# Optimization experiments

Measured on AMD Instinct MI355X. Metric: run time of the kernel, lower is better.

Reference implementation:

```python
import jax, jax.numpy as jnp
import numpy as np

T, B, E, H, R, NHASH, CHUNK = 2048, 2, 1024, 8, 2, 8, 32
D = E // H
INF = 1.0e16  # module's self.inf
BIG = 1.0e8   # module's self.big


def setup_inputs() -> dict:
    key = jax.random.key(0)
    ks = jax.random.split(key, 8)
    w = lambda k, shape, s=0.02: jax.random.normal(k, shape, dtype=jnp.float32) * s
    return {
        "query": jax.random.normal(ks[0], (T, B, E), jnp.float32),
        "key":   jax.random.normal(ks[1], (T, B, E), jnp.float32),
        "value": jax.random.normal(ks[2], (T, B, E), jnp.float32),
        "Wq": w(ks[3], (E, E)), "bq": jnp.zeros((E,), jnp.float32),
        "Wv": w(ks[4], (E, E)), "bv": jnp.zeros((E,), jnp.float32),
        "Wo": w(ks[5], (E, E)), "bo": jnp.zeros((E,), jnp.float32),
        "hash_w": w(ks[6], (R, H, D, NHASH // 2), 0.1),
    }


def _hashes(x_tbhd, hash_w):
    # einsum('ibnf,rnfh->ibrnh'), cat([lin,-lin]), argmax -> [T,B,R,H]
    lin = jnp.einsum('tbhd,rhdn->tbrhn', x_tbhd, hash_w)
    return jnp.argmax(jnp.concatenate([lin, -lin], axis=-1), axis=-1)


def _gather_t(x_bhtd, perm_brht):
    # gather along T with per-(b,r,h) permutation -> [B,R,H,T,D]
    Bb, Rr, Hh, Tt = perm_brht.shape
    Dd = x_bhtd.shape[-1]
    xb = jnp.broadcast_to(x_bhtd[:, None], (Bb, Rr, Hh, Tt, Dd))
    idx = jnp.broadcast_to(perm_brht[..., None], (Bb, Rr, Hh, Tt, Dd))
    return jnp.take_along_axis(xb, idx, axis=3)


def reference(query, key, value, Wq, bq, Wv, bv, Wo, bo, hash_w):
    del key  # share_kq=True (self-attention): keys are L2-normalized queries
    scaling = D ** -0.5
    qf = query @ Wq + bq                                    # [T,B,E]
    kf = qf / jnp.linalg.norm(qf, axis=-1, keepdims=True)   # F.normalize over embed dim
    vf = value @ Wv + bv
    q = qf.reshape(T, B, H, D) * scaling
    k = kf.reshape(T, B, H, D)
    v = vf.reshape(T, B, H, D)

    q_hash = _hashes(q, hash_w)                             # [T,B,R,H]
    k_hash = _hashes(k, hash_w)

    qh_t = jnp.transpose(q_hash, (1, 2, 3, 0))              # [B,R,H,T]
    kh_t = jnp.transpose(k_hash, (1, 2, 3, 0))
    p_q = jnp.argsort(qh_t, axis=-1)                        # stable sort by hash
    p_k = jnp.argsort(kh_t, axis=-1)
    inv_q = jnp.argsort(p_q, axis=-1)                       # sorted position of each token

    q_s = _gather_t(jnp.transpose(q, (1, 2, 0, 3)), p_q)    # [B,R,H,T,D]
    k_s = _gather_t(jnp.transpose(k, (1, 2, 0, 3)), p_k)
    v_s = _gather_t(jnp.transpose(v, (1, 2, 0, 3)), p_k)
    qh_s = jnp.take_along_axis(qh_t, p_q, axis=-1)
    kh_s = jnp.take_along_axis(kh_t, p_k, axis=-1)

    C = T // CHUNK
    M = 3 * CHUNK
    chunk = lambda x: x.reshape(x.shape[:3] + (C, CHUNK) + x.shape[4:])
    q_c, qh_c, qid_c = chunk(q_s), chunk(qh_s), chunk(p_q)
    k_c, v_c, kh_c, kid_c = chunk(k_s), chunk(v_s), chunk(kh_s), chunk(p_k)

    # each query chunk attends key chunks {c-1, c, c+1} (num_chunk_offsets=3, wraparound)
    blocks = lambda x: jnp.concatenate([jnp.roll(x, 1, axis=3), x, jnp.roll(x, -1, axis=3)], axis=4)
    kb, vb, khb, kidb = blocks(k_c), blocks(v_c), blocks(kh_c), blocks(kid_c)

    scores = jnp.einsum('brhcld,brhcmd->brhclm', q_c, kb)   # q pre-scaled by d^-0.5
    scores = scores - INF * (qh_c[..., :, None] != khb[..., None, :])   # mask_different_hashes
    scores = scores - BIG * (qid_c[..., :, None] == kidb[..., None, :]) # mask_current

    # cross-round duplicate counting: key ids attended per original query
    chunk_of = inv_q // CHUNK                               # [B,R,H,T]
    idx = jnp.broadcast_to(chunk_of[..., None], (B, R, H, T, M))
    A = jnp.take_along_axis(kidb, idx, axis=3)              # [B,R,H,T,M]
    dup = []
    for r in range(R):
        c = jnp.zeros((B, H, T, M), jnp.int32)
        for r2 in range(R):
            c = c + (A[:, r, :, :, :, None] == A[:, r2, :, :, None, :]).sum(-1, dtype=jnp.int32)
        dup.append(c)
    dup = jnp.stack(dup, axis=1)                            # [B,R,H,T,M]
    idx2 = jnp.broadcast_to(p_q[..., None], (B, R, H, T, M))
    dup_s = jnp.take_along_axis(dup, idx2, axis=3)          # sorted-query order
    scores = scores - jnp.log(dup_s.astype(scores.dtype)).reshape(scores.shape)

    z = jax.nn.logsumexp(scores, axis=-1)                   # [B,R,H,C,L]
    attn = jax.nn.softmax(scores, axis=-1)
    o = jnp.einsum('brhclm,brhcmd->brhcld', attn, vb).reshape(B, R, H, T, D)
    z = z.reshape(B, R, H, T)

    # scatter back to original token order
    idx3 = jnp.broadcast_to(inv_q[..., None], (B, R, H, T, D))
    o = jnp.take_along_axis(o, idx3, axis=3)
    z = jnp.take_along_axis(z, inv_q, axis=3)

    w = jax.nn.softmax(z, axis=1)                           # combine rounds by logsumexp weight
    out = (w[..., None] * o).sum(axis=1)                    # [B,H,T,D]
    out = jnp.transpose(out, (2, 0, 1, 3)).reshape(T, B, E)
    return out @ Wo + bo
```

## Files before the change

### kernel.cpp

```cpp
#include <hip/hip_runtime.h>

typedef unsigned short ushort_t;
typedef __bf16 bf16x8 __attribute__((ext_vector_type(8)));
typedef float f32x4 __attribute__((ext_vector_type(4)));

#define T_DIM 2048
#define B_DIM 2
#define E_DIM 1024
#define H_DIM 8
#define R_DIM 2
#define D_DIM 128
#define M_WIN 96
#define SCALING 0.08838834764831845f
#define LN2F 0.69314718055994530942f

__device__ __forceinline__ float bfu(unsigned u) {
  union { unsigned i; float f; } x; x.i = u << 16; return x.f;
}
__device__ __forceinline__ unsigned f2bf(float f) {
  union { float f; unsigned i; } x; x.f = f;
  unsigned r = x.i + 0x7fffu + ((x.i >> 16) & 1u);
  return r >> 16;
}
__device__ __forceinline__ void gl_lds16(const void* g, void* l) {
  __builtin_amdgcn_global_load_lds(
      (const __attribute__((address_space(1))) unsigned int*)g,
      (__attribute__((address_space(3))) unsigned int*)l, 16, 0, 0);
}

__global__ __launch_bounds__(256) void packA_kernel(const float* __restrict__ q,
                                                    const float* __restrict__ v,
                                                    ushort_t* __restrict__ qh,
                                                    ushort_t* __restrict__ vh)
{
  int bid = blockIdx.x;
  const float* src = (bid < 4096) ? q : v;
  ushort_t* dst = (bid < 4096) ? qh : vh;
  int i = ((bid & 4095) * 256 + threadIdx.x) * 4;
  float4 x = *(const float4*)&src[i];
  uint2 oh;
  oh.x = f2bf(x.x) | (f2bf(x.y) << 16);
  oh.y = f2bf(x.z) | (f2bf(x.w) << 16);
  *(uint2*)&dst[i] = oh;
}

__global__ __launch_bounds__(256) void packT_kernel(
    const float* __restrict__ w0, const float* __restrict__ w1,
    const float* __restrict__ w2, ushort_t* __restrict__ o0,
    ushort_t* __restrict__ o1, ushort_t* __restrict__ o2)
{
  const float* in = (blockIdx.z == 0) ? w0 : (blockIdx.z == 1) ? w1 : w2;
  ushort_t* hi = (blockIdx.z == 0) ? o0 : (blockIdx.z == 1) ? o1 : o2;
  __shared__ float tile[64][65];
  const int tid = threadIdx.x;
  const int k0 = blockIdx.y * 64, n0 = blockIdx.x * 64;
  const int tr = tid >> 4, tc4 = (tid & 15) * 4;
#pragma unroll
  for (int rr = 0; rr < 64; rr += 16)
    *(float4*)&tile[tr + rr][tc4] = *(const float4*)&in[(size_t)(k0 + tr + rr) * E_DIM + n0 + tc4];
  __syncthreads();
#pragma unroll
  for (int rr = 0; rr < 64; rr += 16) {
    int n = n0 + tr + rr;
    uint2 oh;
    oh.x = f2bf(tile[tc4 + 0][tr + rr]) | (f2bf(tile[tc4 + 1][tr + rr]) << 16);
    oh.y = f2bf(tile[tc4 + 2][tr + rr]) | (f2bf(tile[tc4 + 3][tr + rr]) << 16);
    *(uint2*)&hi[(size_t)n * E_DIM + k0 + tc4] = oh;
  }
}

__global__ __launch_bounds__(256) void fuseF_kernel(const float* __restrict__ Wq,
                                                    const float* __restrict__ bq,
                                                    const float* __restrict__ hw,
                                                    float* __restrict__ F,
                                                    float* __restrict__ cvec)
{
  __shared__ float wl[512];
  const int rh = blockIdx.x, h = rh & 7;
  const int tid = threadIdx.x;
  for (int i = tid; i < 512; i += 256) wl[i] = hw[rh * 512 + i];
  __syncthreads();
  for (int e = tid; e < E_DIM; e += 256) {
    const float* wr = Wq + (size_t)e * E_DIM + h * D_DIM;
    float a0 = 0.f, a1 = 0.f, a2 = 0.f, a3 = 0.f;
    for (int d = 0; d < 128; d += 4) {
      float4 q4 = *(const float4*)&wr[d];
      float4 w0 = *(const float4*)&wl[d * 4];
      float4 w1 = *(const float4*)&wl[d * 4 + 4];
      float4 w2 = *(const float4*)&wl[d * 4 + 8];
      float4 w3 = *(const float4*)&wl[d * 4 + 12];
      a0 += q4.x * w0.x + q4.y * w1.x + q4.z * w2.x + q4.w * w3.x;
      a1 += q4.x * w0.y + q4.y * w1.y + q4.z * w2.y + q4.w * w3.y;
      a2 += q4.x * w0.z + q4.y * w1.z + q4.z * w2.z + q4.w * w3.z;
      a3 += q4.x * w0.w + q4.y * w1.w + q4.z * w2.w + q4.w * w3.w;
    }
    float4 o; o.x = a0; o.y = a1; o.z = a2; o.w = a3;
    *(float4*)&F[(size_t)e * 64 + rh * 4] = o;
  }
  if (tid < 4) {
    float acc = 0.f;
    for (int d = 0; d < 128; ++d) acc += bq[h * D_DIM + d] * wl[d * 4 + tid];
    cvec[rh * 4 + tid] = acc;
  }
}

__global__ __launch_bounds__(256) void hashlin_kernel(const float* __restrict__ query,
                                                      const float* __restrict__ F,
                                                      const float* __restrict__ cvec,
                                                      int* __restrict__ hashb)
{
  __shared__ float As[32][17];
  __shared__ float Fs[32][64];
  const int tid = threadIdx.x;
  const int ty = tid >> 4, tx = tid & 15;
  const int r0 = blockIdx.x * 16;
  float acc0 = 0.f, acc1 = 0.f, acc2 = 0.f, acc3 = 0.f;
  for (int k0 = 0; k0 < E_DIM; k0 += 32) {
    __syncthreads();
    {
      int i = tid * 2, row = i >> 5, kk = i & 31;
      float2 a2 = *(const float2*)&query[(size_t)(r0 + row) * E_DIM + k0 + kk];
      As[kk][row] = a2.x; As[kk + 1][row] = a2.y;
    }
    {
      int i = tid * 8, kk = i >> 6, cc = i & 63;
      float4 f0 = *(const float4*)&F[(size_t)(k0 + kk) * 64 + cc];
      float4 f1 = *(const float4*)&F[(size_t)(k0 + kk) * 64 + cc + 4];
      *(float4*)&Fs[kk][cc] = f0;
      *(float4*)&Fs[kk][cc + 4] = f1;
    }
    __syncthreads();
#pragma unroll
    for (int kk = 0; kk < 32; ++kk) {
      float a = As[kk][ty];
      float4 f4 = *(const float4*)&Fs[kk][tx * 4];
      acc0 += a * f4.x; acc1 += a * f4.y; acc2 += a * f4.z; acc3 += a * f4.w;
    }
  }
  float4 c4 = *(const float4*)&cvec[tx * 4];
  float lin[4] = {acc0 + c4.x, acc1 + c4.y, acc2 + c4.z, acc3 + c4.w};
  float best = lin[0]; int bi = 0;
#pragma unroll
  for (int idx = 1; idx < 8; ++idx) {
    float v = (idx < 4) ? lin[idx] : -lin[idx - 4];
    if (v > best) { best = v; bi = idx; }
  }
  int grow = r0 + ty;
  int t = grow >> 1, b = grow & 1;
  int rr = tx >> 3, hh = tx & 7;
  hashb[(size_t)((b * R_DIM + rr) * H_DIM + hh) * T_DIM + t] = bi;
}

__global__ __launch_bounds__(256) void gemm_mfma(
    const ushort_t* __restrict__ A0, const ushort_t* __restrict__ B0,
    const float* __restrict__ bias0, float* __restrict__ C0,
    const ushort_t* __restrict__ A1, const ushort_t* __restrict__ B1,
    const float* __restrict__ bias1, float* __restrict__ C1)
{
  const ushort_t* Ah = blockIdx.z ? A1 : A0;
  const ushort_t* Bh = blockIdx.z ? B1 : B0;
  const float* bias = blockIdx.z ? bias1 : bias0;
  float* C = blockIdx.z ? C1 : C0;

  __shared__ ushort_t As[128 * 32];
  __shared__ ushort_t Bs[64 * 32];
  const int tid = threadIdx.x;
  const int w = tid >> 6, lane = tid & 63;
  const int lm = lane & 15, quad = lane >> 4;
  const int wr = w >> 1, wc = w & 1;
  const int m0 = blockIdx.y * 128, n0 = blockIdx.x * 64;

  f32x4 acc[4][2] = {};

  for (int k0 = 0; k0 < E_DIM; k0 += 32) {
    __syncthreads();
#pragma unroll
    for (int j = 0; j < 2; ++j) {
      int g = j * 256 + w * 64 + lane;
      gl_lds16(Ah + (size_t)(m0 + (g >> 2)) * E_DIM + k0 + (g & 3) * 8,
               &As[(size_t)(j * 256 + w * 64) * 8]);
    }
    {
      int g = w * 64 + lane;
      gl_lds16(Bh + (size_t)(n0 + (g >> 2)) * E_DIM + k0 + (g & 3) * 8,
               &Bs[(size_t)(w * 64) * 8]);
    }
    __syncthreads();

    bf16x8 av[4], bv[2];
#pragma unroll
    for (int i = 0; i < 4; ++i) av[i] = *(const bf16x8*)&As[(wr * 64 + i * 16 + lm) * 32 + quad * 8];
#pragma unroll
    for (int j = 0; j < 2; ++j) bv[j] = *(const bf16x8*)&Bs[(wc * 32 + j * 16 + lm) * 32 + quad * 8];
#pragma unroll
    for (int i = 0; i < 4; ++i)
#pragma unroll
      for (int j = 0; j < 2; ++j)
        acc[i][j] = __builtin_amdgcn_mfma_f32_16x16x32_bf16(av[i], bv[j], acc[i][j], 0, 0, 0);
  }

#pragma unroll
  for (int j = 0; j < 2; ++j) {
    int col = n0 + wc * 32 + j * 16 + lm;
    float bj = bias[col];
#pragma unroll
    for (int i = 0; i < 4; ++i)
#pragma unroll
      for (int rg = 0; rg < 4; ++rg)
        C[(size_t)(m0 + wr * 64 + i * 16 + quad * 4 + rg) * E_DIM + col] = acc[i][j][rg] + bj;
  }
}

__global__ __launch_bounds__(256) void norm_kernel(const float* __restrict__ qf,
                                                   float* __restrict__ inv_nrm)
{
  int row = blockIdx.x, tid = threadIdx.x;
  const float* r = qf + (size_t)row * E_DIM;
  float4 v = *(const float4*)(r + tid * 4);
  float s = v.x * v.x + v.y * v.y + v.z * v.z + v.w * v.w;
  for (int off = 1; off < 64; off <<= 1) s += __shfl_xor(s, off);
  __shared__ float part[4];
  if ((tid & 63) == 0) part[tid >> 6] = s;
  __syncthreads();
  if (tid == 0) {
    float t = part[0] + part[1] + part[2] + part[3];
    inv_nrm[row] = 1.0f / sqrtf(t);
  }
}

__global__ __launch_bounds__(256) void sort_kernel(const int* __restrict__ hashb,
                                                   int* __restrict__ p, int* __restrict__ inv)
{
  const int bid = blockIdx.x, tid = threadIdx.x;
  const int lane = tid & 63, w = tid >> 6;
  const int* hrow = hashb + (size_t)bid * T_DIM;
  __shared__ int mat[8][256];
  __shared__ int btot[8], bbase[8];
  int cnt[8];
#pragma unroll
  for (int v = 0; v < 8; ++v) cnt[v] = 0;
  int hv[8];
#pragma unroll
  for (int j = 0; j < 8; ++j) { hv[j] = hrow[tid * 8 + j]; cnt[hv[j]]++; }
#pragma unroll
  for (int v = 0; v < 8; ++v) mat[v][tid] = cnt[v];
  __syncthreads();
  for (int v = w; v < 8; v += 4) {
    int4 c4 = *(const int4*)&mat[v][lane * 4];
    int s = c4.x + c4.y + c4.z + c4.w;
    int x = s;
    for (int off = 1; off < 64; off <<= 1) {
      int y = __shfl_up(x, off);
      if (lane >= off) x += y;
    }
    int excl = x - s;
    mat[v][lane * 4 + 0] = excl;
    mat[v][lane * 4 + 1] = excl + c4.x;
    mat[v][lane * 4 + 2] = excl + c4.x + c4.y;
    mat[v][lane * 4 + 3] = excl + c4.x + c4.y + c4.z;
    if (lane == 63) btot[v] = x;
  }
  __syncthreads();
  if (tid == 0) {
    int run = 0;
    for (int v = 0; v < 8; ++v) { bbase[v] = run; run += btot[v]; }
  }
  __syncthreads();
#pragma unroll
  for (int v = 0; v < 8; ++v) cnt[v] = 0;
#pragma unroll
  for (int j = 0; j < 8; ++j) {
    int v = hv[j];
    int pos = bbase[v] + mat[v][tid] + cnt[v];
    cnt[v]++;
    p[(size_t)bid * T_DIM + pos] = tid * 8 + j;
    inv[(size_t)bid * T_DIM + tid * 8 + j] = pos;
  }
}

__global__ __launch_bounds__(256) void attn_kernel(
    const float* __restrict__ qf, const float* __restrict__ vf,
    const float* __restrict__ inv_nrm, const int* __restrict__ hashb,
    const int* __restrict__ p, const int* __restrict__ inv,
    ushort_t* __restrict__ o_out, float* __restrict__ z_out)
{
  const int c = blockIdx.x, h = blockIdx.y, bz = blockIdx.z;
  const int b = bz >> 1, r = bz & 1;
  const int brh = (b * R_DIM + r) * H_DIM + h;
  const int brh_o = (b * R_DIM + (r ^ 1)) * H_DIM + h;
  const int tid = threadIdx.x;
  const int lane = tid & 63, w = tid >> 6;
  const int lm = lane & 15, quad = lane >> 4;

  __shared__ __align__(16) unsigned char smem[39424];
  ushort_t* Qs = (ushort_t*)smem;
  ushort_t* Ks = (ushort_t*)(smem + 8704);
  ushort_t* VT = (ushort_t*)smem;
  float*    SS = (float*)(smem + 26624);
  ushort_t* Ps = (ushort_t*)(smem + 26624);
  __shared__ int skp[M_WIN], sqp[32];
  __shared__ float s_invn[M_WIN];

  if (tid < M_WIN) {
    int m = tid;
    int chunk = (c + (m >> 5) + 63) & 63;
    int pos = chunk * 32 + (m & 31);
    int t = p[(size_t)brh * T_DIM + pos];
    int hh = hashb[(size_t)brh * T_DIM + t];
    int co = inv[(size_t)brh_o * T_DIM + t] >> 5;
    skp[m] = t | (hh << 11) | (co << 14);
    s_invn[m] = inv_nrm[t * B_DIM + b];
    if (m < 32) {
      int tq = p[(size_t)brh * T_DIM + c * 32 + m];
      int qh = hashb[(size_t)brh * T_DIM + tq];
      int qco = inv[(size_t)brh_o * T_DIM + tq] >> 5;
      sqp[m] = tq | (qh << 11) | (qco << 14);
    }
  }
  __syncthreads();

  for (int idx = tid; idx < 1024; idx += 256) {
    int row = idx >> 5, seg = idx & 31;
    int t = sqp[row] & 2047;
    float4 v = *(const float4*)(qf + ((size_t)(t * B_DIM + b) << 10) + h * D_DIM + seg * 4);
    uint2 o2;
    o2.x = f2bf(v.x * SCALING) | (f2bf(v.y * SCALING) << 16);
    o2.y = f2bf(v.z * SCALING) | (f2bf(v.w * SCALING) << 16);
    *(uint2*)&Qs[row * 136 + seg * 4] = o2;
  }
  for (int idx = tid; idx < 3072; idx += 256) {
    int m = idx >> 5, seg = idx & 31;
    int t = skp[m] & 2047;
    float inrm = s_invn[m];
    float4 v = *(const float4*)(qf + ((size_t)(t * B_DIM + b) << 10) + h * D_DIM + seg * 4);
    uint2 o2;
    o2.x = f2bf(v.x * inrm) | (f2bf(v.y * inrm) << 16);
    o2.y = f2bf(v.z * inrm) | (f2bf(v.w * inrm) << 16);
    *(uint2*)&Ks[m * 136 + seg * 4] = o2;
  }
  __syncthreads();

  const int mw = w & 1, nset = w >> 1;
  bf16x8 av[4];
#pragma unroll
  for (int kk = 0; kk < 4; ++kk)
    av[kk] = *(const bf16x8*)&Qs[(mw * 16 + lm) * 136 + kk * 32 + quad * 8];
  f32x4 sacc[3] = {};
#pragma unroll
  for (int jj = 0; jj < 3; ++jj) {
    int nt = nset * 3 + jj;
#pragma unroll
    for (int kk = 0; kk < 4; ++kk) {
      bf16x8 bv = *(const bf16x8*)&Ks[(nt * 16 + lm) * 136 + kk * 32 + quad * 8];
      sacc[jj] = __builtin_amdgcn_mfma_f32_16x16x32_bf16(av[kk], bv, sacc[jj], 0, 0, 0);
    }
  }
  __syncthreads();

  const int rowb = mw * 16 + quad * 4;
#pragma unroll
  for (int jj = 0; jj < 3; ++jj) {
    int col = (nset * 3 + jj) * 16 + lm;
    int kp = skp[col];
#pragma unroll
    for (int rg = 0; rg < 4; ++rg) {
      int qp = sqp[rowb + rg];
      float sc = sacc[jj][rg];
      if ((kp ^ qp) & 0x3800) sc -= 1.0e16f;
      if (!((kp ^ qp) & 0x7FF)) sc -= 1.0e8f;
      int dc = ((kp >> 14) - (qp >> 14)) & 63;
      if (dc <= 1 || dc == 63) sc -= LN2F;
      SS[(rowb + rg) * 100 + col] = sc;
    }
  }
  for (int idx = tid; idx < 3072; idx += 256) {
    int d = idx & 127, mg = idx >> 7;
    int t0 = skp[mg * 4 + 0] & 2047, t1 = skp[mg * 4 + 1] & 2047;
    int t2 = skp[mg * 4 + 2] & 2047, t3 = skp[mg * 4 + 3] & 2047;
    const size_t off = (size_t)h * D_DIM + d;
    unsigned vv0 = f2bf(vf[((size_t)(t0 * B_DIM + b) << 10) + off]);
    unsigned vv1 = f2bf(vf[((size_t)(t1 * B_DIM + b) << 10) + off]);
    unsigned vv2 = f2bf(vf[((size_t)(t2 * B_DIM + b) << 10) + off]);
    unsigned vv3 = f2bf(vf[((size_t)(t3 * B_DIM + b) << 10) + off]);
    uint2 o2; o2.x = vv0 | (vv1 << 16); o2.y = vv2 | (vv3 << 16);
    *(uint2*)&VT[d * 104 + mg * 4] = o2;
  }
  __syncthreads();

  {
    const int l = tid >> 3, g = tid & 7;
    float smy[12];
#pragma unroll
    for (int j = 0; j < 12; ++j) smy[j] = SS[l * 100 + g + 8 * j];
    float mx = smy[0];
#pragma unroll
    for (int j = 1; j < 12; ++j) mx = fmaxf(mx, smy[j]);
    mx = fmaxf(mx, __shfl_xor(mx, 1));
    mx = fmaxf(mx, __shfl_xor(mx, 2));
    mx = fmaxf(mx, __shfl_xor(mx, 4));
    float sum = 0.f, ey[12];
#pragma unroll
    for (int j = 0; j < 12; ++j) { ey[j] = expf(smy[j] - mx); sum += ey[j]; }
    sum += __shfl_xor(sum, 1);
    sum += __shfl_xor(sum, 2);
    sum += __shfl_xor(sum, 4);
    float inv_s = 1.0f / sum;
#pragma unroll
    for (int j = 0; j < 12; ++j)
      Ps[l * 200 + g + 8 * j] = (ushort_t)f2bf(ey[j] * inv_s);
    if (g == 0) z_out[(size_t)brh * T_DIM + (sqp[l] & 2047)] = mx + logf(sum);
  }
  __syncthreads();

  const int dset = w >> 1;
  bf16x8 pa[3];
#pragma unroll
  for (int kk = 0; kk < 3; ++kk)
    pa[kk] = *(const bf16x8*)&Ps[(mw * 16 + lm) * 200 + kk * 32 + quad * 8];
  f32x4 oacc[4] = {};
#pragma unroll
  for (int jj = 0; jj < 4; ++jj) {
    int dt = dset * 4 + jj;
#pragma unroll
    for (int kk = 0; kk < 3; ++kk) {
      bf16x8 bv = *(const bf16x8*)&VT[(dt * 16 + lm) * 104 + kk * 32 + quad * 8];
      oacc[jj] = __builtin_amdgcn_mfma_f32_16x16x32_bf16(pa[kk], bv, oacc[jj], 0, 0, 0);
    }
  }
#pragma unroll
  for (int jj = 0; jj < 4; ++jj) {
    int col = (dset * 4 + jj) * 16 + lm;
#pragma unroll
    for (int rg = 0; rg < 4; ++rg) {
      int tqo = sqp[rowb + rg] & 2047;
      o_out[((size_t)brh * T_DIM + tqo) * D_DIM + col] = (ushort_t)f2bf(oacc[jj][rg]);
    }
  }
}

__global__ __launch_bounds__(256) void combine_kernel(const ushort_t* __restrict__ obf,
                                                      const float* __restrict__ z_buf,
                                                      ushort_t* __restrict__ ctx)
{
  int gid = blockIdx.x * 256 + threadIdx.x;
  int d4 = gid & 31;
  int t = (gid >> 5) & (T_DIM - 1);
  int h = (gid >> 16) & 7;
  int b = gid >> 19;
  int brh0 = (b * R_DIM + 0) * H_DIM + h;
  int brh1 = brh0 + H_DIM;
  float z0 = z_buf[(size_t)brh0 * T_DIM + t], z1 = z_buf[(size_t)brh1 * T_DIM + t];
  float mz = fmaxf(z0, z1);
  float e0 = expf(z0 - mz), e1 = expf(z1 - mz);
  float is = 1.0f / (e0 + e1);
  float w0 = e0 * is, w1 = e1 * is;
  uint2 a = *(const uint2*)&obf[((size_t)brh0 * T_DIM + t) * D_DIM + d4 * 4];
  uint2 cc = *(const uint2*)&obf[((size_t)brh1 * T_DIM + t) * D_DIM + d4 * 4];
  uint2 o;
  o.x = f2bf(w0 * bfu(a.x & 0xffffu) + w1 * bfu(cc.x & 0xffffu)) |
        (f2bf(w0 * bfu(a.x >> 16) + w1 * bfu(cc.x >> 16)) << 16);
  o.y = f2bf(w0 * bfu(a.y & 0xffffu) + w1 * bfu(cc.y & 0xffffu)) |
        (f2bf(w0 * bfu(a.y >> 16) + w1 * bfu(cc.y >> 16)) << 16);
  *(uint2*)&ctx[((size_t)(t * B_DIM + b) << 10) + h * D_DIM + d4 * 4] = o;
}

extern "C" void kernel_launch(void* const* d_in, const int* in_sizes, int n_in,
                              void* d_out, int out_size, void* d_ws, size_t ws_size,
                              hipStream_t stream)
{
  const float* query = (const float*)d_in[0];
  const float* value = (const float*)d_in[2];
  const float* Wq = (const float*)d_in[3];
  const float* bq = (const float*)d_in[4];
  const float* Wv = (const float*)d_in[5];
  const float* bv = (const float*)d_in[6];
  const float* Wo = (const float*)d_in[7];
  const float* bo = (const float*)d_in[8];
  const float* hw = (const float*)d_in[9];

  float* ws = (float*)d_ws;
  float* qf   = ws;
  float* vf   = qf + 4194304;
  float* bigf = vf + 4194304;
  ushort_t* obuf = (ushort_t*)bigf;
  ushort_t* ctx  = obuf + 8388608;
  ushort_t* qh   = (ushort_t*)bigf;
  ushort_t* vh   = qh + 4194304;
  ushort_t* WqTh = (ushort_t*)(bigf + 6291456);
  ushort_t* WvTh = WqTh + 1048576;
  ushort_t* WoTh = WvTh + 1048576;
  float* F       = (float*)(WoTh + 1048576);
  float* cvec    = F + 65536;
  float* zbuf    = cvec + 64;
  float* inv_nrm = zbuf + 65536;
  int*   hashb   = (int*)(inv_nrm + 4096);
  int*   pperm   = hashb + 65536;
  int*   pinv    = pperm + 65536;

  packA_kernel<<<8192, 256, 0, stream>>>(query, value, qh, vh);
  packT_kernel<<<dim3(16, 16, 3), 256, 0, stream>>>(Wq, Wv, Wo, WqTh, WvTh, WoTh);
  fuseF_kernel<<<16, 256, 0, stream>>>(Wq, bq, hw, F, cvec);
  hashlin_kernel<<<256, 256, 0, stream>>>(query, F, cvec, hashb);
  gemm_mfma<<<dim3(16, 32, 2), 256, 0, stream>>>(qh, WqTh, bq, qf, vh, WvTh, bv, vf);
  norm_kernel<<<4096, 256, 0, stream>>>(qf, inv_nrm);
  sort_kernel<<<32, 256, 0, stream>>>(hashb, pperm, pinv);
  attn_kernel<<<dim3(64, 8, 4), 256, 0, stream>>>(qf, vf, inv_nrm, hashb, pperm, pinv, obuf, zbuf);
  combine_kernel<<<4096, 256, 0, stream>>>(obuf, zbuf, ctx);
  gemm_mfma<<<dim3(16, 32, 1), 256, 0, stream>>>(ctx, WoTh, bo, (float*)d_out,
                                                 (ushort_t*)nullptr, (ushort_t*)nullptr,
                                                 (const float*)nullptr, (float*)nullptr);
}
```

Before: 272.3 us.

## Store projections in bf16, pre-gather sorted K/V, merge small kernels, widen GEMM tile

The three prep kernels are merged into one launch, and norm and sort are merged into another. The Q/V projection GEMM now writes bf16 outputs, and its N tile grows from 64 to 128. A new gather kernel writes hash-sorted K rows and transposed V chunks once. The attention kernel then streams them with direct global-to-LDS loads and reuses the centre K chunk as Q, applying the scaling and inverse norm to the scores. The aim is to cut fp32 traffic, the repeated per-window gathers and the launch count, at the cost of an extra intermediate buffer, higher register pressure in the GEMM and bf16 rounding of Q before normalisation.

New measurement: 283.1 us. 1.04x slower.

```diff
diff --git a/kernel.cpp b/kernel.cpp
--- a/kernel.cpp
+++ b/kernel.cpp
@@ -28,79 +28,73 @@
       (__attribute__((address_space(3))) unsigned int*)l, 16, 0, 0);
 }
 
-__global__ __launch_bounds__(256) void packA_kernel(const float* __restrict__ q,
-                                                    const float* __restrict__ v,
-                                                    ushort_t* __restrict__ qh,
-                                                    ushort_t* __restrict__ vh)
-{
-  int bid = blockIdx.x;
-  const float* src = (bid < 4096) ? q : v;
-  ushort_t* dst = (bid < 4096) ? qh : vh;
-  int i = ((bid & 4095) * 256 + threadIdx.x) * 4;
-  float4 x = *(const float4*)&src[i];
-  uint2 oh;
-  oh.x = f2bf(x.x) | (f2bf(x.y) << 16);
-  oh.y = f2bf(x.z) | (f2bf(x.w) << 16);
-  *(uint2*)&dst[i] = oh;
-}
-
-__global__ __launch_bounds__(256) void packT_kernel(
-    const float* __restrict__ w0, const float* __restrict__ w1,
-    const float* __restrict__ w2, ushort_t* __restrict__ o0,
-    ushort_t* __restrict__ o1, ushort_t* __restrict__ o2)
-{
-  const float* in = (blockIdx.z == 0) ? w0 : (blockIdx.z == 1) ? w1 : w2;
-  ushort_t* hi = (blockIdx.z == 0) ? o0 : (blockIdx.z == 1) ? o1 : o2;
-  __shared__ float tile[64][65];
-  const int tid = threadIdx.x;
-  const int k0 = blockIdx.y * 64, n0 = blockIdx.x * 64;
-  const int tr = tid >> 4, tc4 = (tid & 15) * 4;
-#pragma unroll
-  for (int rr = 0; rr < 64; rr += 16)
-    *(float4*)&tile[tr + rr][tc4] = *(const float4*)&in[(size_t)(k0 + tr + rr) * E_DIM + n0 + tc4];
-  __syncthreads();
-#pragma unroll
-  for (int rr = 0; rr < 64; rr += 16) {
-    int n = n0 + tr + rr;
+__global__ __launch_bounds__(256) void prep_kernel(
+    const float* __restrict__ query, const float* __restrict__ value,
+    const float* __restrict__ Wq, const float* __restrict__ Wv,
+    const float* __restrict__ Wo, const float* __restrict__ bq,
+    const float* __restrict__ hw,
+    ushort_t* __restrict__ qh, ushort_t* __restrict__ vh,
+    ushort_t* __restrict__ WqT, ushort_t* __restrict__ WvT,
+    ushort_t* __restrict__ WoT, float* __restrict__ F, float* __restrict__ cvec)
+{
+  __shared__ float plds[4160];
+  const int bid = blockIdx.x, tid = threadIdx.x;
+  if (bid < 8192) {
+    const float* src = (bid < 4096) ? query : value;
+    ushort_t* dst = (bid < 4096) ? qh : vh;
+    int i = ((bid & 4095) * 256 + tid) * 4;
+    float4 x = *(const float4*)&src[i];
     uint2 oh;
-    oh.x = f2bf(tile[tc4 + 0][tr + rr]) | (f2bf(tile[tc4 + 1][tr + rr]) << 16);
-    oh.y = f2bf(tile[tc4 + 2][tr + rr]) | (f2bf(tile[tc4 + 3][tr + rr]) << 16);
-    *(uint2*)&hi[(size_t)n * E_DIM + k0 + tc4] = oh;
-  }
-}
-
-__global__ __launch_bounds__(256) void fuseF_kernel(const float* __restrict__ Wq,
-                                                    const float* __restrict__ bq,
-                                                    const float* __restrict__ hw,
-                                                    float* __restrict__ F,
-                                                    float* __restrict__ cvec)
-{
-  __shared__ float wl[512];
-  const int rh = blockIdx.x, h = rh & 7;
-  const int tid = threadIdx.x;
-  for (int i = tid; i < 512; i += 256) wl[i] = hw[rh * 512 + i];
-  __syncthreads();
-  for (int e = tid; e < E_DIM; e += 256) {
-    const float* wr = Wq + (size_t)e * E_DIM + h * D_DIM;
-    float a0 = 0.f, a1 = 0.f, a2 = 0.f, a3 = 0.f;
-    for (int d = 0; d < 128; d += 4) {
-      float4 q4 = *(const float4*)&wr[d];
-      float4 w0 = *(const float4*)&wl[d * 4];
-      float4 w1 = *(const float4*)&wl[d * 4 + 4];
-      float4 w2 = *(const float4*)&wl[d * 4 + 8];
-      float4 w3 = *(const float4*)&wl[d * 4 + 12];
-      a0 += q4.x * w0.x + q4.y * w1.x + q4.z * w2.x + q4.w * w3.x;
-      a1 += q4.x * w0.y + q4.y * w1.y + q4.z * w2.y + q4.w * w3.y;
-      a2 += q4.x * w0.z + q4.y * w1.z + q4.z * w2.z + q4.w * w3.z;
-      a3 += q4.x * w0.w + q4.y * w1.w + q4.z * w2.w + q4.w * w3.w;
-    }
-    float4 o; o.x = a0; o.y = a1; o.z = a2; o.w = a3;
-    *(float4*)&F[(size_t)e * 64 + rh * 4] = o;
-  }
-  if (tid < 4) {
-    float acc = 0.f;
-    for (int d = 0; d < 128; ++d) acc += bq[h * D_DIM + d] * wl[d * 4 + tid];
-    cvec[rh * 4 + tid] = acc;
+    oh.x = f2bf(x.x) | (f2bf(x.y) << 16);
+    oh.y = f2bf(x.z) | (f2bf(x.w) << 16);
+    *(uint2*)&dst[i] = oh;
+  } else if (bid < 8960) {
+    int idx = bid - 8192;
+    const float* in = (idx < 256) ? Wq : (idx < 512) ? Wv : Wo;
+    ushort_t* hi = (idx < 256) ? WqT : (idx < 512) ? WvT : WoT;
+    int tile = idx & 255;
+    int n0 = (tile & 15) * 64, k0 = (tile >> 4) * 64;
+    float (*t64)[65] = (float(*)[65])plds;
+    const int tr = tid >> 4, tc4 = (tid & 15) * 4;
+#pragma unroll
+    for (int rr = 0; rr < 64; rr += 16)
+      *(float4*)&t64[tr + rr][tc4] = *(const float4*)&in[(size_t)(k0 + tr + rr) * E_DIM + n0 + tc4];
+    __syncthreads();
+#pragma unroll
+    for (int rr = 0; rr < 64; rr += 16) {
+      int n = n0 + tr + rr;
+      uint2 oh;
+      oh.x = f2bf(t64[tc4 + 0][tr + rr]) | (f2bf(t64[tc4 + 1][tr + rr]) << 16);
+      oh.y = f2bf(t64[tc4 + 2][tr + rr]) | (f2bf(t64[tc4 + 3][tr + rr]) << 16);
+      *(uint2*)&hi[(size_t)n * E_DIM + k0 + tc4] = oh;
+    }
+  } else {
+    float* wl = plds;
+    const int rh = bid - 8960, h = rh & 7;
+    for (int i = tid; i < 512; i += 256) wl[i] = hw[rh * 512 + i];
+    __syncthreads();
+    for (int e = tid; e < E_DIM; e += 256) {
+      const float* wr = Wq + (size_t)e * E_DIM + h * D_DIM;
+      float a0 = 0.f, a1 = 0.f, a2 = 0.f, a3 = 0.f;
+      for (int d = 0; d < 128; d += 4) {
+        float4 q4 = *(const float4*)&wr[d];
+        float4 w0 = *(const float4*)&wl[d * 4];
+        float4 w1 = *(const float4*)&wl[d * 4 + 4];
+        float4 w2 = *(const float4*)&wl[d * 4 + 8];
+        float4 w3 = *(const float4*)&wl[d * 4 + 12];
+        a0 += q4.x * w0.x + q4.y * w1.x + q4.z * w2.x + q4.w * w3.x;
+        a1 += q4.x * w0.y + q4.y * w1.y + q4.z * w2.y + q4.w * w3.y;
+        a2 += q4.x * w0.z + q4.y * w1.z + q4.z * w2.z + q4.w * w3.z;
+        a3 += q4.x * w0.w + q4.y * w1.w + q4.z * w2.w + q4.w * w3.w;
+      }
+      float4 o; o.x = a0; o.y = a1; o.z = a2; o.w = a3;
+      *(float4*)&F[(size_t)e * 64 + rh * 4] = o;
+    }
+    if (tid < 4) {
+      float acc = 0.f;
+      for (int d = 0; d < 128; ++d) acc += bq[h * D_DIM + d] * wl[d * 4 + tid];
+      cvec[rh * 4 + tid] = acc;
+    }
   }
 }
 
@@ -153,89 +147,90 @@
 
 __global__ __launch_bounds__(256) void gemm_mfma(
     const ushort_t* __restrict__ A0, const ushort_t* __restrict__ B0,
-    const float* __restrict__ bias0, float* __restrict__ C0,
+    const float* __restrict__ bias0, ushort_t* __restrict__ Cb0, float* __restrict__ Cf0,
     const ushort_t* __restrict__ A1, const ushort_t* __restrict__ B1,
-    const float* __restrict__ bias1, float* __restrict__ C1)
+    const float* __restrict__ bias1, ushort_t* __restrict__ Cb1, float* __restrict__ Cf1)
 {
   const ushort_t* Ah = blockIdx.z ? A1 : A0;
   const ushort_t* Bh = blockIdx.z ? B1 : B0;
   const float* bias = blockIdx.z ? bias1 : bias0;
-  float* C = blockIdx.z ? C1 : C0;
+  ushort_t* Cb = blockIdx.z ? Cb1 : Cb0;
+  float* Cf = blockIdx.z ? Cf1 : Cf0;
 
   __shared__ ushort_t As[128 * 32];
-  __shared__ ushort_t Bs[64 * 32];
-  const int tid = threadIdx.x;
-  const int w = tid >> 6, lane = tid & 63;
+  __shared__ ushort_t Bs[128 * 32];
+  const int tid = threadIdx.x, w = tid >> 6, lane = tid & 63;
   const int lm = lane & 15, quad = lane >> 4;
   const int wr = w >> 1, wc = w & 1;
-  const int m0 = blockIdx.y * 128, n0 = blockIdx.x * 64;
-
-  f32x4 acc[4][2] = {};
+  const int m0 = blockIdx.y * 128, n0 = blockIdx.x * 128;
+  const int lrow = lane >> 2, lcol = (lane & 3) * 8;
+
+  f32x4 acc[4][4] = {};
 
   for (int k0 = 0; k0 < E_DIM; k0 += 32) {
     __syncthreads();
 #pragma unroll
-    for (int j = 0; j < 2; ++j) {
-      int g = j * 256 + w * 64 + lane;
-      gl_lds16(Ah + (size_t)(m0 + (g >> 2)) * E_DIM + k0 + (g & 3) * 8,
-               &As[(size_t)(j * 256 + w * 64) * 8]);
-    }
-    {
-      int g = w * 64 + lane;
-      gl_lds16(Bh + (size_t)(n0 + (g >> 2)) * E_DIM + k0 + (g & 3) * 8,
-               &Bs[(size_t)(w * 64) * 8]);
-    }
-    __syncthreads();
-
-    bf16x8 av[4], bv[2];
+    for (int k = 0; k < 8; ++k) {
+      if ((k & 3) == w) {
+        gl_lds16(Ah + (size_t)(m0 + k * 16 + lrow) * E_DIM + k0 + lcol, &As[k * 512]);
+        gl_lds16(Bh + (size_t)(n0 + k * 16 + lrow) * E_DIM + k0 + lcol, &Bs[k * 512]);
+      }
+    }
+    __syncthreads();
+    bf16x8 av[4], bv[4];
 #pragma unroll
     for (int i = 0; i < 4; ++i) av[i] = *(const bf16x8*)&As[(wr * 64 + i * 16 + lm) * 32 + quad * 8];
 #pragma unroll
-    for (int j = 0; j < 2; ++j) bv[j] = *(const bf16x8*)&Bs[(wc * 32 + j * 16 + lm) * 32 + quad * 8];
+    for (int j = 0; j < 4; ++j) bv[j] = *(const bf16x8*)&Bs[(wc * 64 + j * 16 + lm) * 32 + quad * 8];
 #pragma unroll
     for (int i = 0; i < 4; ++i)
 #pragma unroll
-      for (int j = 0; j < 2; ++j)
+      for (int j = 0; j < 4; ++j)
         acc[i][j] = __builtin_amdgcn_mfma_f32_16x16x32_bf16(av[i], bv[j], acc[i][j], 0, 0, 0);
   }
-
-#pragma unroll
-  for (int j = 0; j < 2; ++j) {
-    int col = n0 + wc * 32 + j * 16 + lm;
+#pragma unroll
+  for (int j = 0; j < 4; ++j) {
+    int col = n0 + wc * 64 + j * 16 + lm;
     float bj = bias[col];
 #pragma unroll
-    for (int i = 0; i < 4; ++i)
-#pragma unroll
-      for (int rg = 0; rg < 4; ++rg)
-        C[(size_t)(m0 + wr * 64 + i * 16 + quad * 4 + rg) * E_DIM + col] = acc[i][j][rg] + bj;
-  }
-}
-
-__global__ __launch_bounds__(256) void norm_kernel(const float* __restrict__ qf,
-                                                   float* __restrict__ inv_nrm)
-{
-  int row = blockIdx.x, tid = threadIdx.x;
-  const float* r = qf + (size_t)row * E_DIM;
-  float4 v = *(const float4*)(r + tid * 4);
-  float s = v.x * v.x + v.y * v.y + v.z * v.z + v.w * v.w;
-  for (int off = 1; off < 64; off <<= 1) s += __shfl_xor(s, off);
+    for (int i = 0; i < 4; ++i) {
+      int rowb = m0 + wr * 64 + i * 16 + quad * 4;
+#pragma unroll
+      for (int rg = 0; rg < 4; ++rg) {
+        float val = acc[i][j][rg] + bj;
+        if (Cb) Cb[(size_t)(rowb + rg) * E_DIM + col] = (ushort_t)f2bf(val);
+        else    Cf[(size_t)(rowb + rg) * E_DIM + col] = val;
+      }
+    }
+  }
+}
+
+__global__ __launch_bounds__(256) void normsort_kernel(
+    const ushort_t* __restrict__ qfb, float* __restrict__ inv_nrm,
+    const int* __restrict__ hashb, int* __restrict__ p, int* __restrict__ inv)
+{
+  __shared__ int mat[8][256];
+  __shared__ int btot[8], bbase[8];
   __shared__ float part[4];
-  if ((tid & 63) == 0) part[tid >> 6] = s;
-  __syncthreads();
-  if (tid == 0) {
-    float t = part[0] + part[1] + part[2] + part[3];
-    inv_nrm[row] = 1.0f / sqrtf(t);
-  }
-}
-
-__global__ __launch_bounds__(256) void sort_kernel(const int* __restrict__ hashb,
-                                                   int* __restrict__ p, int* __restrict__ inv)
-{
-  const int bid = blockIdx.x, tid = threadIdx.x;
+  const int tid = threadIdx.x;
+  if (blockIdx.x < 4096) {
+    int row = blockIdx.x;
+    uint2 u = *(const uint2*)&qfb[((size_t)row << 10) + tid * 4];
+    float a0 = bfu(u.x & 0xffffu), a1 = bfu(u.x >> 16);
+    float a2 = bfu(u.y & 0xffffu), a3 = bfu(u.y >> 16);
+    float s = a0 * a0 + a1 * a1 + a2 * a2 + a3 * a3;
+    for (int off = 1; off < 64; off <<= 1) s += __shfl_xor(s, off);
+    if ((tid & 63) == 0) part[tid >> 6] = s;
+    __syncthreads();
+    if (tid == 0) {
+      float t = part[0] + part[1] + part[2] + part[3];
+      inv_nrm[row] = 1.0f / sqrtf(t);
+    }
+    return;
+  }
+  const int bid = blockIdx.x - 4096;
   const int lane = tid & 63, w = tid >> 6;
   const int* hrow = hashb + (size_t)bid * T_DIM;
-  __shared__ int mat[8][256];
-  __shared__ int btot[8], bbase[8];
   int cnt[8];
 #pragma unroll
   for (int v = 0; v < 8; ++v) cnt[v] = 0;
@@ -278,65 +273,109 @@
   }
 }
 
-__global__ __launch_bounds__(256) void attn_kernel(
-    const float* __restrict__ qf, const float* __restrict__ vf,
+__global__ __launch_bounds__(256) void gather_kernel(
+    const ushort_t* __restrict__ qfb, const ushort_t* __restrict__ vfb,
     const float* __restrict__ inv_nrm, const int* __restrict__ hashb,
     const int* __restrict__ p, const int* __restrict__ inv,
+    int* __restrict__ meta_s, float* __restrict__ invn_s,
+    ushort_t* __restrict__ ksort, ushort_t* __restrict__ vt)
+{
+  const int c = blockIdx.x, brh = blockIdx.y;
+  const int b = brh >> 4, h = brh & 7;
+  const int brh_o = brh ^ 8;
+  const int tid = threadIdx.x;
+  __shared__ int ts[32];
+  __shared__ ushort_t vtile[32 * 136];
+
+  if (tid < 32) {
+    int pos = c * 32 + tid;
+    int t = p[(size_t)brh * T_DIM + pos];
+    int hh = hashb[(size_t)brh * T_DIM + t];
+    int co = inv[(size_t)brh_o * T_DIM + t] >> 5;
+    meta_s[(size_t)brh * T_DIM + pos] = t | (hh << 11) | (co << 14);
+    invn_s[(size_t)brh * T_DIM + pos] = inv_nrm[t * B_DIM + b];
+    ts[tid] = t;
+  }
+  __syncthreads();
+  {
+    int i = tid >> 3, part = tid & 7;
+    int t = ts[i];
+    const ushort_t* src = qfb + ((size_t)(t * B_DIM + b) << 10) + h * D_DIM + part * 16;
+    uint4 a = *(const uint4*)src;
+    uint4 bb = *(const uint4*)(src + 8);
+    ushort_t* dst = ksort + ((size_t)brh * T_DIM + c * 32 + i) * 136 + part * 16;
+    *(uint4*)dst = a; *(uint4*)(dst + 8) = bb;
+    const ushort_t* vsrc = vfb + ((size_t)(t * B_DIM + b) << 10) + h * D_DIM + part * 16;
+    uint4 va = *(const uint4*)vsrc;
+    uint4 vb = *(const uint4*)(vsrc + 8);
+    ushort_t* vdst = &vtile[i * 136 + part * 16];
+    *(uint4*)vdst = va; *(uint4*)(vdst + 8) = vb;
+  }
+  __syncthreads();
+  {
+    int d = tid >> 1, half = tid & 1;
+    unsigned pk[8];
+#pragma unroll
+    for (int jj = 0; jj < 8; ++jj) {
+      unsigned lo = vtile[(half * 16 + jj * 2) * 136 + d];
+      unsigned hi = vtile[(half * 16 + jj * 2 + 1) * 136 + d];
+      pk[jj] = lo | (hi << 16);
+    }
+    ushort_t* out = vt + ((size_t)(brh * 64 + c)) * 4096 + d * 32 + half * 16;
+    uint4 o0; o0.x = pk[0]; o0.y = pk[1]; o0.z = pk[2]; o0.w = pk[3];
+    uint4 o1; o1.x = pk[4]; o1.y = pk[5]; o1.z = pk[6]; o1.w = pk[7];
+    *(uint4*)out = o0; *(uint4*)(out + 8) = o1;
+  }
+}
+
+__global__ __launch_bounds__(256) void attn_kernel(
+    const ushort_t* __restrict__ ksort, const ushort_t* __restrict__ vt,
+    const int* __restrict__ meta_s, const float* __restrict__ invn_s,
     ushort_t* __restrict__ o_out, float* __restrict__ z_out)
 {
   const int c = blockIdx.x, h = blockIdx.y, bz = blockIdx.z;
   const int b = bz >> 1, r = bz & 1;
   const int brh = (b * R_DIM + r) * H_DIM + h;
-  const int brh_o = (b * R_DIM + (r ^ 1)) * H_DIM + h;
   const int tid = threadIdx.x;
   const int lane = tid & 63, w = tid >> 6;
   const int lm = lane & 15, quad = lane >> 4;
 
-  __shared__ __align__(16) unsigned char smem[39424];
-  ushort_t* Qs = (ushort_t*)smem;
-  ushort_t* Ks = (ushort_t*)(smem + 8704);
-  ushort_t* VT = (ushort_t*)smem;
-  float*    SS = (float*)(smem + 26624);
-  ushort_t* Ps = (ushort_t*)(smem + 26624);
-  __shared__ int skp[M_WIN], sqp[32];
+  __shared__ __align__(16) unsigned char smem[50688];
+  ushort_t* Kw = (ushort_t*)smem;
+  ushort_t* VTb = (ushort_t*)(smem + 26112);
+  float*    SS = (float*)smem;
+  ushort_t* Ps = (ushort_t*)(smem + 13312);
+  __shared__ int skp[M_WIN];
   __shared__ float s_invn[M_WIN];
 
+  int cjs[3] = {(c + 63) & 63, c, (c + 1) & 63};
+
+  int cnt = 0;
+#pragma unroll
+  for (int j = 0; j < 3; ++j) {
+    const ushort_t* gk = ksort + ((size_t)brh * T_DIM + cjs[j] * 32) * 136;
+    ushort_t* lk = Kw + j * 4352;
+#pragma unroll
+    for (int k = 0; k < 8; ++k) {
+      if ((cnt++ & 3) == w) gl_lds16(gk + k * 512 + lane * 8, lk + k * 512);
+    }
+    if ((cnt++ & 3) == w) {
+      if (lane < 32) gl_lds16(gk + 4096 + lane * 8, lk + 4096);
+    }
+  }
+#pragma unroll
+  for (int j = 0; j < 3; ++j) {
+    const ushort_t* gv = vt + ((size_t)(brh * 64 + cjs[j])) * 4096;
+    ushort_t* lv = VTb + j * 4096;
+#pragma unroll
+    for (int k = 0; k < 8; ++k) {
+      if ((cnt++ & 3) == w) gl_lds16(gv + k * 512 + lane * 8, lv + k * 512);
+    }
+  }
   if (tid < M_WIN) {
-    int m = tid;
-    int chunk = (c + (m >> 5) + 63) & 63;
-    int pos = chunk * 32 + (m & 31);
-    int t = p[(size_t)brh * T_DIM + pos];
-    int hh = hashb[(size_t)brh * T_DIM + t];
-    int co = inv[(size_t)brh_o * T_DIM + t] >> 5;
-    skp[m] = t | (hh << 11) | (co << 14);
-    s_invn[m] = inv_nrm[t * B_DIM + b];
-    if (m < 32) {
-      int tq = p[(size_t)brh * T_DIM + c * 32 + m];
-      int qh = hashb[(size_t)brh * T_DIM + tq];
-      int qco = inv[(size_t)brh_o * T_DIM + tq] >> 5;
-      sqp[m] = tq | (qh << 11) | (qco << 14);
-    }
-  }
-  __syncthreads();
-
-  for (int idx = tid; idx < 1024; idx += 256) {
-    int row = idx >> 5, seg = idx & 31;
-    int t = sqp[row] & 2047;
-    float4 v = *(const float4*)(qf + ((size_t)(t * B_DIM + b) << 10) + h * D_DIM + seg * 4);
-    uint2 o2;
-    o2.x = f2bf(v.x * SCALING) | (f2bf(v.y * SCALING) << 16);
-    o2.y = f2bf(v.z * SCALING) | (f2bf(v.w * SCALING) << 16);
-    *(uint2*)&Qs[row * 136 + seg * 4] = o2;
-  }
-  for (int idx = tid; idx < 3072; idx += 256) {
-    int m = idx >> 5, seg = idx & 31;
-    int t = skp[m] & 2047;
-    float inrm = s_invn[m];
-    float4 v = *(const float4*)(qf + ((size_t)(t * B_DIM + b) << 10) + h * D_DIM + seg * 4);
-    uint2 o2;
-    o2.x = f2bf(v.x * inrm) | (f2bf(v.y * inrm) << 16);
-    o2.y = f2bf(v.z * inrm) | (f2bf(v.w * inrm) << 16);
-    *(uint2*)&Ks[m * 136 + seg * 4] = o2;
+    int pos = cjs[tid >> 5] * 32 + (tid & 31);
+    skp[tid] = meta_s[(size_t)brh * T_DIM + pos];
+    s_invn[tid] = invn_s[(size_t)brh * T_DIM + pos];
   }
   __syncthreads();
 
@@ -344,14 +383,14 @@
   bf16x8 av[4];
 #pragma unroll
   for (int kk = 0; kk < 4; ++kk)
-    av[kk] = *(const bf16x8*)&Qs[(mw * 16 + lm) * 136 + kk * 32 + quad * 8];
+    av[kk] = *(const bf16x8*)&Kw[(32 + mw * 16 + lm) * 136 + kk * 32 + quad * 8];
   f32x4 sacc[3] = {};
 #pragma unroll
   for (int jj = 0; jj < 3; ++jj) {
     int nt = nset * 3 + jj;
 #pragma unroll
     for (int kk = 0; kk < 4; ++kk) {
-      bf16x8 bv = *(const bf16x8*)&Ks[(nt * 16 + lm) * 136 + kk * 32 + quad * 8];
+      bf16x8 bv = *(const bf16x8*)&Kw[(nt * 16 + lm) * 136 + kk * 32 + quad * 8];
       sacc[jj] = __builtin_amdgcn_mfma_f32_16x16x32_bf16(av[kk], bv, sacc[jj], 0, 0, 0);
     }
   }
@@ -362,10 +401,11 @@
   for (int jj = 0; jj < 3; ++jj) {
     int col = (nset * 3 + jj) * 16 + lm;
     int kp = skp[col];
+    float scl = SCALING * s_invn[col];
 #pragma unroll
     for (int rg = 0; rg < 4; ++rg) {
-      int qp = sqp[rowb + rg];
-      float sc = sacc[jj][rg];
+      int qp = skp[32 + rowb + rg];
+      float sc = sacc[jj][rg] * scl;
       if ((kp ^ qp) & 0x3800) sc -= 1.0e16f;
       if (!((kp ^ qp) & 0x7FF)) sc -= 1.0e8f;
       int dc = ((kp >> 14) - (qp >> 14)) & 63;
@@ -373,18 +413,6 @@
       SS[(rowb + rg) * 100 + col] = sc;
     }
   }
-  for (int idx = tid; idx < 3072; idx += 256) {
-    int d = idx & 127, mg = idx >> 7;
-    int t0 = skp[mg * 4 + 0] & 2047, t1 = skp[mg * 4 + 1] & 2047;
-    int t2 = skp[mg * 4 + 2] & 2047, t3 = skp[mg * 4 + 3] & 2047;
-    const size_t off = (size_t)h * D_DIM + d;
-    unsigned vv0 = f2bf(vf[((size_t)(t0 * B_DIM + b) << 10) + off]);
-    unsigned vv1 = f2bf(vf[((size_t)(t1 * B_DIM + b) << 10) + off]);
-    unsigned vv2 = f2bf(vf[((size_t)(t2 * B_DIM + b) << 10) + off]);
-    unsigned vv3 = f2bf(vf[((size_t)(t3 * B_DIM + b) << 10) + off]);
-    uint2 o2; o2.x = vv0 | (vv1 << 16); o2.y = vv2 | (vv3 << 16);
-    *(uint2*)&VT[d * 104 + mg * 4] = o2;
-  }
   __syncthreads();
 
   {
@@ -407,8 +435,8 @@
     float inv_s = 1.0f / sum;
 #pragma unroll
     for (int j = 0; j < 12; ++j)
-      Ps[l * 200 + g + 8 * j] = (ushort_t)f2bf(ey[j] * inv_s);
-    if (g == 0) z_out[(size_t)brh * T_DIM + (sqp[l] & 2047)] = mx + logf(sum);
+      Ps[l * 104 + g + 8 * j] = (ushort_t)f2bf(ey[j] * inv_s);
+    if (g == 0) z_out[(size_t)brh * T_DIM + (skp[32 + l] & 2047)] = mx + logf(sum);
   }
   __syncthreads();
 
@@ -416,14 +444,15 @@
   bf16x8 pa[3];
 #pragma unroll
   for (int kk = 0; kk < 3; ++kk)
-    pa[kk] = *(const bf16x8*)&Ps[(mw * 16 + lm) * 200 + kk * 32 + quad * 8];
+    pa[kk] = *(const bf16x8*)&Ps[(mw * 16 + lm) * 104 + kk * 32 + quad * 8];
   f32x4 oacc[4] = {};
 #pragma unroll
   for (int jj = 0; jj < 4; ++jj) {
     int dt = dset * 4 + jj;
 #pragma unroll
     for (int kk = 0; kk < 3; ++kk) {
-      bf16x8 bv = *(const bf16x8*)&VT[(dt * 16 + lm) * 104 + kk * 32 + quad * 8];
+      const ushort_t* VTk = VTb + kk * 4096;
+      bf16x8 bv = *(const bf16x8*)&VTk[(dt * 16 + lm) * 32 + quad * 8];
       oacc[jj] = __builtin_amdgcn_mfma_f32_16x16x32_bf16(pa[kk], bv, oacc[jj], 0, 0, 0);
     }
   }
@@ -432,7 +461,7 @@
     int col = (dset * 4 + jj) * 16 + lm;
 #pragma unroll
     for (int rg = 0; rg < 4; ++rg) {
-      int tqo = sqp[rowb + rg] & 2047;
+      int tqo = skp[32 + rowb + rg] & 2047;
       o_out[((size_t)brh * T_DIM + tqo) * D_DIM + col] = (ushort_t)f2bf(oacc[jj][rg]);
     }
   }
@@ -479,34 +508,38 @@
   const float* hw = (const float*)d_in[9];
 
   float* ws = (float*)d_ws;
-  float* qf   = ws;
-  float* vf   = qf + 4194304;
-  float* bigf = vf + 4194304;
-  ushort_t* obuf = (ushort_t*)bigf;
-  ushort_t* ctx  = obuf + 8388608;
-  ushort_t* qh   = (ushort_t*)bigf;
-  ushort_t* vh   = qh + 4194304;
-  ushort_t* WqTh = (ushort_t*)(bigf + 6291456);
-  ushort_t* WvTh = WqTh + 1048576;
-  ushort_t* WoTh = WvTh + 1048576;
-  float* F       = (float*)(WoTh + 1048576);
-  float* cvec    = F + 65536;
-  float* zbuf    = cvec + 64;
-  float* inv_nrm = zbuf + 65536;
-  int*   hashb   = (int*)(inv_nrm + 4096);
-  int*   pperm   = hashb + 65536;
-  int*   pinv    = pperm + 65536;
-
-  packA_kernel<<<8192, 256, 0, stream>>>(query, value, qh, vh);
-  packT_kernel<<<dim3(16, 16, 3), 256, 0, stream>>>(Wq, Wv, Wo, WqTh, WvTh, WoTh);
-  fuseF_kernel<<<16, 256, 0, stream>>>(Wq, bq, hw, F, cvec);
+  ushort_t* qh    = (ushort_t*)ws;
+  ushort_t* vh    = qh + 4194304;
+  ushort_t* obuf  = qh;
+  ushort_t* qfb   = (ushort_t*)(ws + 4194304);
+  ushort_t* ctx   = qfb;
+  ushort_t* vfb   = qfb + 4194304;
+  ushort_t* ksort = vfb + 4194304;
+  ushort_t* vt    = ksort + 8912896;
+  ushort_t* WqTh  = vt + 8388608;
+  ushort_t* WvTh  = WqTh + 1048576;
+  ushort_t* WoTh  = WvTh + 1048576;
+  float* F        = (float*)(WoTh + 1048576);
+  float* cvec     = F + 65536;
+  float* zbuf     = cvec + 64;
+  float* inv_nrm  = zbuf + 65536;
+  int* hashb      = (int*)(inv_nrm + 4096);
+  int* pperm      = hashb + 65536;
+  int* pinv       = pperm + 65536;
+  int* meta_s     = pinv + 65536;
+  float* invn_s   = (float*)(meta_s + 65536);
+
+  prep_kernel<<<8976, 256, 0, stream>>>(query, value, Wq, Wv, Wo, bq, hw,
+                                        qh, vh, WqTh, WvTh, WoTh, F, cvec);
   hashlin_kernel<<<256, 256, 0, stream>>>(query, F, cvec, hashb);
-  gemm_mfma<<<dim3(16, 32, 2), 256, 0, stream>>>(qh, WqTh, bq, qf, vh, WvTh, bv, vf);
-  norm_kernel<<<4096, 256, 0, stream>>>(qf, inv_nrm);
-  sort_kernel<<<32, 256, 0, stream>>>(hashb, pperm, pinv);
-  attn_kernel<<<dim3(64, 8, 4), 256, 0, stream>>>(qf, vf, inv_nrm, hashb, pperm, pinv, obuf, zbuf);
+  gemm_mfma<<<dim3(8, 32, 2), 256, 0, stream>>>(qh, WqTh, bq, qfb, (float*)nullptr,
+                                                vh, WvTh, bv, vfb, (float*)nullptr);
+  normsort_kernel<<<4128, 256, 0, stream>>>(qfb, inv_nrm, hashb, pperm, pinv);
+  gather_kernel<<<dim3(64, 32), 256, 0, stream>>>(qfb, vfb, inv_nrm, hashb, pperm, pinv,
+                                                  meta_s, invn_s, ksort, vt);
+  attn_kernel<<<dim3(64, 8, 4), 256, 0, stream>>>(ksort, vt, meta_s, invn_s, obuf, zbuf);
   combine_kernel<<<4096, 256, 0, stream>>>(obuf, zbuf, ctx);
-  gemm_mfma<<<dim3(16, 32, 1), 256, 0, stream>>>(ctx, WoTh, bo, (float*)d_out,
-                                                 (ushort_t*)nullptr, (ushort_t*)nullptr,
-                                                 (const float*)nullptr, (float*)nullptr);
-}
+  gemm_mfma<<<dim3(8, 32, 1), 256, 0, stream>>>(ctx, WoTh, bo, (ushort_t*)nullptr, (float*)d_out,
+                                                (const ushort_t*)nullptr, (const ushort_t*)nullptr,
+                                                (const float*)nullptr, (ushort_t*)nullptr, (float*)nullptr);
+}
```
